# Performance work log

Measured on AMD Instinct MI355X. Metric: run time of the kernel, lower is better.

Reference implementation:

```python
import jax, jax.numpy as jnp
import numpy as np


def setup_inputs() -> dict:
    key = jax.random.key(0)
    k1, k2, k3 = jax.random.split(key, 3)
    B, T = 4, 4096
    n_blocks, bs, rem = 1024, 4, 3
    n = n_blocks * bs + rem  # 4099 = min(n, m); full last-dim size
    x = jax.random.normal(k1, (B, T, n), dtype=jnp.float32)
    # matches torch init: 0.1 * randn
    blocks = 0.1 * jax.random.normal(k2, (n_blocks, bs, bs), dtype=jnp.float32)
    diag_remainder = 0.1 * jax.random.normal(k3, (rem,), dtype=jnp.float32)
    return {"x": x, "blocks": blocks, "diag_remainder": diag_remainder, "n": n}


def reference(x, blocks, diag_remainder, n):
    # BlockCore.apply_to_vector: y = D @ x where D is block-diagonal
    # (dense block_size x block_size blocks) plus a diagonal remainder.
    n_blocks, bs, _ = blocks.shape
    block_region_end = n_blocks * bs
    r = diag_remainder.shape[0]
    batch_shape = x.shape[:-1]

    # block region: [..., n_blocks, bs]; y_j = sum_k blocks[b][j,k] * x_k
    xb = x[..., :block_region_end].reshape(*batch_shape, n_blocks, bs)
    y_blocks = jnp.einsum('...nk,njk->...nj', xb, blocks)
    y_blocks = y_blocks.reshape(*batch_shape, block_region_end)

    # remainder diagonal: elementwise multiply
    y_rem = x[..., block_region_end:block_region_end + r] * diag_remainder

    y = jnp.concatenate([y_blocks, y_rem], axis=-1)
    if y.shape[-1] < n:  # zero-pad up to n (static shapes)
        pad = jnp.zeros((*batch_shape, n - y.shape[-1]), dtype=x.dtype)
        y = jnp.concatenate([y, pad], axis=-1)
    return y
```

## Files before the change

kernel.cpp:

```cpp
#include <hip/hip_runtime.h>

constexpr int ROW      = 4099;
constexpr int ROWS     = 16384;
constexpr int GCH      = 64;
constexpr int NGCH     = 1024 / GCH;
constexpr int RCH      = 128;
constexpr int NRCH     = ROWS / RCH;

__global__ __launch_bounds__(256) void blockcore_main(
    const float* __restrict__ x,
    const float* __restrict__ blocks,
    float* __restrict__ y)
{
    const int gchunk = blockIdx.x & (NGCH - 1);
    const int rchunk = blockIdx.x >> 4;
    const int t = threadIdx.x;
    const int q = t >> 2;
    const int j = t & 3;
    const int g = gchunk * GCH + q;

    const float4 b = *reinterpret_cast<const float4*>(blocks + (size_t)g * 16 + (size_t)j * 4);

    const float* xp = x + (size_t)rchunk * RCH * ROW + (size_t)4 * g;
    float*       yp = y + (size_t)rchunk * RCH * ROW + (size_t)4 * g + j;

    #pragma unroll 4
    for (int r = 0; r < RCH; ++r) {
        const float x0 = xp[0];
        const float x1 = xp[1];
        const float x2 = xp[2];
        const float x3 = xp[3];
        *yp = b.x * x0 + b.y * x1 + b.z * x2 + b.w * x3;
        xp += ROW;
        yp += ROW;
    }
}

__global__ __launch_bounds__(256) void blockcore_rem(
    const float* __restrict__ x,
    const float* __restrict__ diag,
    float* __restrict__ y)
{
    const int idx = blockIdx.x * 256 + threadIdx.x;
    if (idx >= ROWS * 3) return;
    const int r = idx / 3;
    const int i = idx - r * 3;
    const size_t off = (size_t)r * ROW + 4096 + i;
    y[off] = x[off] * diag[i];
}

extern "C" void kernel_launch(void* const* d_in, const int* in_sizes, int n_in,
                              void* d_out, int out_size, void* d_ws, size_t ws_size,
                              hipStream_t stream) {
    const float* x      = (const float*)d_in[0];
    const float* blocks = (const float*)d_in[1];
    const float* diag   = (const float*)d_in[2];
    float*       y      = (float*)d_out;

    blockcore_main<<<dim3(NGCH * NRCH), dim3(256), 0, stream>>>(x, blocks, y);
    blockcore_rem<<<dim3((ROWS * 3 + 255) / 256), dim3(256), 0, stream>>>(x, diag, y);
}
```

Baseline: 466.0 us.

## Fuse remainder into main kernel and stage unaligned rows through LDS with float4 loads

Replaces the two kernels with one fused kernel in which each workgroup handles four consecutive rows. The first row is read directly with aligned float4 loads. The remaining three rows plus the first row's remainder form a 16-byte aligned window, which is loaded with float4 into LDS, transformed in place (4x4 blocks and diagonal remainder), and written back with float4 stores. This is meant to replace the strided scalar global accesses with coalesced vector traffic and to remove the second launch, at the cost of about 49KB of LDS per workgroup, which limits occupancy.

Result: slower. 492.1 us (+5.6%).

```diff
diff --git a/kernel.cpp b/kernel.cpp
--- a/kernel.cpp
+++ b/kernel.cpp
@@ -1,52 +1,71 @@
 #include <hip/hip_runtime.h>
 
-constexpr int ROW      = 4099;
-constexpr int ROWS     = 16384;
-constexpr int GCH      = 64;
-constexpr int NGCH     = 1024 / GCH;
-constexpr int RCH      = 128;
-constexpr int NRCH     = ROWS / RCH;
+constexpr int NROW = 16384;
+constexpr int ROWF = 4099;
+constexpr int TR   = 4;
+constexpr int NWG  = NROW / TR;
+constexpr int WIN  = 3 * ROWF + 3;
 
-__global__ __launch_bounds__(256) void blockcore_main(
+__global__ __launch_bounds__(256) void blockcore_fused(
     const float* __restrict__ x,
     const float* __restrict__ blocks,
-    float* __restrict__ y)
-{
-    const int gchunk = blockIdx.x & (NGCH - 1);
-    const int rchunk = blockIdx.x >> 4;
-    const int t = threadIdx.x;
-    const int q = t >> 2;
-    const int j = t & 3;
-    const int g = gchunk * GCH + q;
-
-    const float4 b = *reinterpret_cast<const float4*>(blocks + (size_t)g * 16 + (size_t)j * 4);
-
-    const float* xp = x + (size_t)rchunk * RCH * ROW + (size_t)4 * g;
-    float*       yp = y + (size_t)rchunk * RCH * ROW + (size_t)4 * g + j;
-
-    #pragma unroll 4
-    for (int r = 0; r < RCH; ++r) {
-        const float x0 = xp[0];
-        const float x1 = xp[1];
-        const float x2 = xp[2];
-        const float x3 = xp[3];
-        *yp = b.x * x0 + b.y * x1 + b.z * x2 + b.w * x3;
-        xp += ROW;
-        yp += ROW;
-    }
-}
-
-__global__ __launch_bounds__(256) void blockcore_rem(
-    const float* __restrict__ x,
     const float* __restrict__ diag,
     float* __restrict__ y)
 {
-    const int idx = blockIdx.x * 256 + threadIdx.x;
-    if (idx >= ROWS * 3) return;
-    const int r = idx / 3;
-    const int i = idx - r * 3;
-    const size_t off = (size_t)r * ROW + 4096 + i;
-    y[off] = x[off] * diag[i];
+    __shared__ float lds[WIN];
+    const int t  = threadIdx.x;
+    const int wg = blockIdx.x;
+    const size_t r0       = (size_t)wg * TR;
+    const size_t start_al = r0 * ROWF + 4096;
+
+    const float4* xw = reinterpret_cast<const float4*>(x + start_al);
+    float4*       lw = reinterpret_cast<float4*>(lds);
+
+    float4 sr[13];
+    #pragma unroll
+    for (int i = 0; i < 12; ++i) sr[i] = xw[t + 256 * i];
+    if (t < 3) sr[12] = xw[3072 + t];
+
+    const int q = t >> 2, j = t & 3;
+    const float* xr0 = x + r0 * ROWF;
+    float*       yr0 = y + r0 * ROWF;
+    #pragma unroll 4
+    for (int i = 0; i < 16; ++i) {
+        const int g = q + 64 * i;
+        const float4 xv = *reinterpret_cast<const float4*>(xr0 + 4 * g);
+        const float4 bv = *reinterpret_cast<const float4*>(blocks + 16 * g + 4 * j);
+        yr0[4 * g + j] = bv.x * xv.x + bv.y * xv.y + bv.z * xv.z + bv.w * xv.w;
+    }
+
+    #pragma unroll
+    for (int i = 0; i < 12; ++i) lw[t + 256 * i] = sr[i];
+    if (t < 3) lw[3072 + t] = sr[12];
+    __syncthreads();
+
+    if (t < 3) lds[t] *= diag[t];
+    for (int it = 0; it < 17; ++it) {
+        const int gg = q + 64 * it;
+        if (gg < 1024) {
+            const float4 bv = *reinterpret_cast<const float4*>(blocks + 16 * gg + 4 * j);
+            #pragma unroll
+            for (int lr = 0; lr < 3; ++lr) {
+                const int base = lr * ROWF + 4 * gg + 3;
+                const float x0 = lds[base + 0], x1 = lds[base + 1];
+                const float x2 = lds[base + 2], x3 = lds[base + 3];
+                lds[base + j] = bv.x * x0 + bv.y * x1 + bv.z * x2 + bv.w * x3;
+            }
+        } else if (gg == 1024 && j < 3) {
+            #pragma unroll
+            for (int lr = 0; lr < 3; ++lr)
+                lds[(lr + 1) * ROWF + j] *= diag[j];
+        }
+    }
+    __syncthreads();
+
+    float4* yw = reinterpret_cast<float4*>(y + start_al);
+    #pragma unroll
+    for (int i = 0; i < 12; ++i) yw[t + 256 * i] = lw[t + 256 * i];
+    if (t < 3) yw[3072 + t] = lw[3072 + t];
 }
 
 extern "C" void kernel_launch(void* const* d_in, const int* in_sizes, int n_in,
@@ -57,6 +76,5 @@
     const float* diag   = (const float*)d_in[2];
     float*       y      = (float*)d_out;
 
-    blockcore_main<<<dim3(NGCH * NRCH), dim3(256), 0, stream>>>(x, blocks, y);
-    blockcore_rem<<<dim3((ROWS * 3 + 255) / 256), dim3(256), 0, stream>>>(x, diag, y);
+    blockcore_fused<<<dim3(NWG), dim3(256), 0, stream>>>(x, blocks, diag, y);
 }
```
